# Kernel tuning notes

Hardware: AMD Instinct MI355X
Metric: run time of the kernel (lower is better)

## Reference

```python
import jax, jax.numpy as jnp
import numpy as np

N_SPK = 2048
M_UTT = 16
D_EMB = 512
EPS = 1e-8  # torch cosine_similarity eps


def setup_inputs() -> dict:
    key = jax.random.key(0)
    k1, = jax.random.split(key, 1)
    speaker_vectors = jax.random.normal(k1, (N_SPK * M_UTT, D_EMB), dtype=jnp.float32)
    return {
        "speaker_vectors": speaker_vectors,
        "w": jnp.float32(10.0),
        "b": jnp.float32(-5.0),
        "speakers": N_SPK,
    }


def _normalize(x):
    # torch.cosine_similarity clamps each norm at eps
    n = jnp.maximum(jnp.linalg.norm(x, axis=-1, keepdims=True), EPS)
    return x / n


def reference(speaker_vectors, w, b, speakers):
    N = speakers
    NM, D = speaker_vectors.shape
    M = NM // N
    v3 = speaker_vectors.reshape(N, M, D)
    ssum = v3.sum(axis=1)                         # [N, D] per-speaker sums
    C = ssum / M                                  # full centroids [N, D]
    C_min = (ssum[:, None, :] - v3) / (M - 1)     # leave-one-out centroids [N, M, D]

    vn = _normalize(speaker_vectors)              # [NM, D]
    # diagonal similarities: cos(C_min[j], v[j]) per utterance j
    S_diag = jnp.sum(_normalize(C_min.reshape(NM, D)) * vn, axis=-1)  # [NM]
    # full similarity matrix via one normalized matmul: [N, NM]
    S_full = _normalize(C) @ vn.T
    # replace each speaker's own block row entries with leave-one-out sims
    col_spk = jnp.arange(NM) // M                 # speaker id of each column
    same = col_spk[None, :] == jnp.arange(N)[:, None]  # [N, NM]
    S = jnp.where(same, S_diag[None, :], S_full)

    # L_j = -(w*S_diag_j + b) + log sum_n exp(w*S[n,j] + b)
    L = -(w * S_diag + b) + jax.nn.logsumexp(w * S + b, axis=0)
    return L.sum()
```

## Files before the change

### kernel.cpp

```cpp
#include <hip/hip_runtime.h>
#include <stdint.h>

#define N_SPK 2048
#define M_UTT 16
#define D_EMB 512
#define NM (N_SPK * M_UTT)
#define FP8_SCALE 16.0f

typedef __attribute__((ext_vector_type(4))) float f32x4;
typedef __attribute__((ext_vector_type(4))) int   i32x4;
typedef __attribute__((ext_vector_type(8))) int   i32x8;

__device__ __forceinline__ void async_copy16(const void* g, void* l) {
    __builtin_amdgcn_global_load_lds(
        (const __attribute__((address_space(1))) unsigned int*)g,
        (__attribute__((address_space(3))) unsigned int*)l,
        16, 0, 0);
}

__device__ __forceinline__ i32x8 ld_frag(const unsigned char* base, int s0) {
    i32x4 lo = *(const i32x4*)(base + s0 * 16);
    i32x4 hi = *(const i32x4*)(base + (s0 ^ 1) * 16);
    return __builtin_shufflevector(lo, hi, 0, 1, 2, 3, 4, 5, 6, 7);
}

__global__ __launch_bounds__(256) void prep_kernel(
    const float* __restrict__ V, const float* __restrict__ wp,
    const float* __restrict__ bp, unsigned char* __restrict__ Cn8,
    unsigned char* __restrict__ vn8, float* __restrict__ dterm,
    float* __restrict__ colsum, float* __restrict__ out)
{
    const int spk = blockIdx.x, t = threadIdx.x;
    const int wave = t >> 6, lane = t & 63;
    const float2* vb = (const float2*)(V + (size_t)spk * (M_UTT * D_EMB));

    __shared__ __align__(16) float red[32][264];
    __shared__ float red2[32];
    __shared__ float invs[M_UTT];
    __shared__ float wred[4];

    if (spk < 128) colsum[spk * 256 + t] = 0.f;
    if (spk == 0 && t == 0) out[0] = 0.f;

    float2 p[M_UTT];
#pragma unroll
    for (int m = 0; m < M_UTT; ++m) p[m] = vb[m * 256 + t];

    float2 ss = make_float2(0.f, 0.f);
#pragma unroll
    for (int m = 0; m < M_UTT; ++m) { ss.x += p[m].x; ss.y += p[m].y; }

    float cnp = ss.x * ss.x + ss.y * ss.y;
#pragma unroll
    for (int off = 32; off > 0; off >>= 1) cnp += __shfl_xor(cnp, off);
    if (lane == 0) wred[wave] = cnp;

#pragma unroll
    for (int m = 0; m < M_UTT; ++m) {
        red[m][t]         = ss.x * p[m].x + ss.y * p[m].y;
        red[m + M_UTT][t] = p[m].x * p[m].x + p[m].y * p[m].y;
    }
    __syncthreads();
    const float cn2 = wred[0] + wred[1] + wred[2] + wred[3];

    {
        const int r = t >> 3, s = t & 7;
        const float4* rp = (const float4*)red;
        float4 a = make_float4(0.f, 0.f, 0.f, 0.f);
#pragma unroll
        for (int k = 0; k < 8; ++k) {
            float4 q = rp[r * 66 + s + 8 * k];
            a.x += q.x; a.y += q.y; a.z += q.z; a.w += q.w;
        }
        float v1 = (a.x + a.y) + (a.z + a.w);
        v1 += __shfl_xor(v1, 1);
        v1 += __shfl_xor(v1, 2);
        v1 += __shfl_xor(v1, 4);
        if (s == 0) red2[r] = v1;
    }
    __syncthreads();

    if (t < M_UTT) {
        const float sv = red2[t], vv = red2[t + M_UTT];
        const float cc = cn2 - 2.f * sv + vv;
        const float cv = sv - vv;
        const float dc = fmaxf(sqrtf(fmaxf(cc, 0.f)) * (1.f / (M_UTT - 1)), 1e-8f) * (M_UTT - 1);
        const float dv = fmaxf(sqrtf(vv), 1e-8f);
        dterm[spk * M_UTT + t] = (*wp) * (cv / (dc * dv)) + (*bp);
        invs[t] = FP8_SCALE / dv;
    }
    __syncthreads();

    const float cs = FP8_SCALE / (M_UTT * fmaxf(sqrtf(cn2) * (1.f / M_UTT), 1e-8f));
    {
        int pk = __builtin_amdgcn_cvt_pk_fp8_f32(ss.x * cs, ss.y * cs, 0, false);
        ((unsigned short*)(Cn8 + (size_t)spk * D_EMB))[t] = (unsigned short)pk;
    }
#pragma unroll
    for (int m = 0; m < M_UTT; ++m) {
        const float iv = invs[m];
        int pk = __builtin_amdgcn_cvt_pk_fp8_f32(p[m].x * iv, p[m].y * iv, 0, false);
        ((unsigned short*)(vn8 + ((size_t)(spk * M_UTT + m)) * D_EMB))[t] = (unsigned short)pk;
    }
}

__global__ __launch_bounds__(256) void gemm_kernel(
    const unsigned char* __restrict__ Cn8, const unsigned char* __restrict__ vn8,
    const float* __restrict__ wp, const float* __restrict__ bp,
    float* __restrict__ colsum)
{
    __shared__ __align__(16) unsigned char As[128 * 256];
    __shared__ __align__(16) unsigned char Bs[128 * 256];
    __shared__ float csum[128];

    const int tid = threadIdx.x;
    const int w = tid >> 6, l = tid & 63;
    const int by = blockIdx.x;
    const int bx = blockIdx.y;
    const float wgt = (*wp) * (1.f / (FP8_SCALE * FP8_SCALE));
    const float bsc = *bp;

    if (tid < 128) csum[tid] = 0.f;

    const int r_l = l >> 4, hh = (l >> 3) & 1, sl8 = l & 7;
    const int g_even = sl8 ^ r_l;
    const size_t rowoff = (size_t)(w * 32 + r_l) * D_EMB + hh * 128;
    const unsigned char* Ab0 = Cn8 + (size_t)(by * 128) * D_EMB + rowoff + g_even * 16;
    const unsigned char* Ab1 = Cn8 + (size_t)(by * 128) * D_EMB + rowoff + (g_even ^ 4) * 16;
    const unsigned char* Bb0 = vn8 + (size_t)(bx * 128) * D_EMB + rowoff + g_even * 16;
    const unsigned char* Bb1 = vn8 + (size_t)(bx * 128) * D_EMB + rowoff + (g_even ^ 4) * 16;
    unsigned char* AsW = As + (w * 32) * 256;
    unsigned char* BsW = Bs + (w * 32) * 256;

    const int wm = w & 1, wn = w >> 1;
    const int l16 = l & 15, q = l >> 4;
    const int s0 = (2 * q) ^ (l & 7);
    const unsigned char* Ard = As + (wm * 64 + l16) * 256;
    const unsigned char* Brd = Bs + (wn * 64 + l16) * 256;

    f32x4 acc[4][4];
    const f32x4 z = {0.f, 0.f, 0.f, 0.f};
#pragma unroll
    for (int i = 0; i < 4; ++i)
#pragma unroll
        for (int j = 0; j < 4; ++j) acc[i][j] = z;

#pragma unroll
    for (int kk = 0; kk < D_EMB; kk += 256) {
        __syncthreads();
#pragma unroll
        for (int i = 0; i < 8; ++i) {
            const unsigned char* pa = ((i & 1) ? Ab1 : Ab0) + i * 2048 + kk;
            const unsigned char* pb = ((i & 1) ? Bb1 : Bb0) + i * 2048 + kk;
            async_copy16(pa, AsW + i * 1024);
            async_copy16(pb, BsW + i * 1024);
        }
        __syncthreads();
#pragma unroll
        for (int h2 = 0; h2 < 2; ++h2) {
            const int ho = h2 * 128;
            i32x8 bfr[4];
#pragma unroll
            for (int j = 0; j < 4; ++j) bfr[j] = ld_frag(Brd + j * 4096 + ho, s0);
#pragma unroll
            for (int i = 0; i < 4; ++i) {
                i32x8 af = ld_frag(Ard + i * 4096 + ho, s0);
#pragma unroll
                for (int j = 0; j < 4; ++j)
                    acc[i][j] = __builtin_amdgcn_mfma_scale_f32_16x16x128_f8f6f4(
                        af, bfr[j], acc[i][j], 0, 0, 0, 0x7F7F7F7F, 0, 0x7F7F7F7F);
            }
        }
    }

    const int rowg0 = by * 128 + wm * 64 + q * 4;
    const int colg0 = bx * 128 + wn * 64 + l16;
#pragma unroll
    for (int j = 0; j < 4; ++j) {
        const int colg = colg0 + j * 16;
        const int cspk = colg >> 4;
        float p = 0.f;
#pragma unroll
        for (int i = 0; i < 4; ++i) {
            const int rowg = rowg0 + i * 16;
#pragma unroll
            for (int r = 0; r < 4; ++r) {
                float e = __expf(wgt * acc[i][j][r] + bsc);
                p += (rowg + r == cspk) ? 0.f : e;
            }
        }
        p += __shfl_xor(p, 16);
        p += __shfl_xor(p, 32);
        if (q == 0) atomicAdd(&csum[wn * 64 + j * 16 + l16], p);
    }
    __syncthreads();
    if (tid < 128) atomicAdd(&colsum[bx * 128 + tid], csum[tid]);
}

__global__ __launch_bounds__(256) void finish_kernel(
    const float* __restrict__ dterm, const float* __restrict__ colsum,
    float* __restrict__ out)
{
    const int idx = blockIdx.x * 256 + threadIdx.x;
    const int stride = gridDim.x * 256;
    float local = 0.f;
    for (int j = idx; j < NM; j += stride) {
        float t = dterm[j];
        local += logf(colsum[j] + __expf(t)) - t;
    }
#pragma unroll
    for (int off = 32; off > 0; off >>= 1) local += __shfl_xor(local, off);
    __shared__ float wr[4];
    const int wave = threadIdx.x >> 6, lane = threadIdx.x & 63;
    if (lane == 0) wr[wave] = local;
    __syncthreads();
    if (threadIdx.x == 0) atomicAdd(out, wr[0] + wr[1] + wr[2] + wr[3]);
}

extern "C" void kernel_launch(void* const* d_in, const int* in_sizes, int n_in,
                              void* d_out, int out_size, void* d_ws, size_t ws_size,
                              hipStream_t stream) {
    const float* V  = (const float*)d_in[0];
    const float* wp = (const float*)d_in[1];
    const float* bp = (const float*)d_in[2];

    char* ws = (char*)d_ws;
    unsigned char* Cn8 = (unsigned char*)ws;
    unsigned char* vn8 = (unsigned char*)(ws + ((size_t)1 << 20));
    float* dterm  = (float*)(ws + ((size_t)17 << 20));
    float* colsum = dterm + NM;
    float* out    = (float*)d_out;

    prep_kernel<<<N_SPK, 256, 0, stream>>>(V, wp, bp, Cn8, vn8, dterm, colsum, out);
    gemm_kernel<<<dim3(N_SPK / 128, NM / 128), 256, 0, stream>>>(Cn8, vn8, wp, bp, colsum);
    finish_kernel<<<64, 256, 0, stream>>>(dterm, colsum, out);
}
```

Baseline: 149.2 us.

## Double-buffer LDS tiles along K in the FP8 GEMM kernel

The GEMM kernel now splits the 512-wide K dimension into four 128-byte stages held in two LDS buffers, instead of two 256-byte stages in a single buffer. The async global-to-LDS copy for the next stage is issued before the MFMA work on the current stage, so loads overlap with compute. The XOR swizzle is rewritten for the 128-byte row stride. In exchange there are more barrier rounds per tile, and correctness depends on the barrier also waiting for the outstanding async copies.

Result: slower. 154.8 us (+3.8%).

```diff
diff --git a/kernel.cpp b/kernel.cpp
--- a/kernel.cpp
+++ b/kernel.cpp
@@ -109,8 +109,8 @@
     const float* __restrict__ wp, const float* __restrict__ bp,
     float* __restrict__ colsum)
 {
-    __shared__ __align__(16) unsigned char As[128 * 256];
-    __shared__ __align__(16) unsigned char Bs[128 * 256];
+    __shared__ __align__(16) unsigned char As[2][128 * 128];
+    __shared__ __align__(16) unsigned char Bs[2][128 * 128];
     __shared__ float csum[128];
 
     const int tid = threadIdx.x;
@@ -122,21 +122,17 @@
 
     if (tid < 128) csum[tid] = 0.f;
 
-    const int r_l = l >> 4, hh = (l >> 3) & 1, sl8 = l & 7;
-    const int g_even = sl8 ^ r_l;
-    const size_t rowoff = (size_t)(w * 32 + r_l) * D_EMB + hh * 128;
-    const unsigned char* Ab0 = Cn8 + (size_t)(by * 128) * D_EMB + rowoff + g_even * 16;
-    const unsigned char* Ab1 = Cn8 + (size_t)(by * 128) * D_EMB + rowoff + (g_even ^ 4) * 16;
-    const unsigned char* Bb0 = vn8 + (size_t)(bx * 128) * D_EMB + rowoff + g_even * 16;
-    const unsigned char* Bb1 = vn8 + (size_t)(bx * 128) * D_EMB + rowoff + (g_even ^ 4) * 16;
-    unsigned char* AsW = As + (w * 32) * 256;
-    unsigned char* BsW = Bs + (w * 32) * 256;
+    const int srow = w * 32 + (l >> 3);
+    const int sg   = (l & 7) ^ ((l >> 3) & 7);
+    const unsigned char* Ab = Cn8 + (size_t)(by * 128 + srow) * D_EMB + sg * 16;
+    const unsigned char* Bb = vn8 + (size_t)(bx * 128 + srow) * D_EMB + sg * 16;
+    const int woff = (w * 32) * 128;
 
     const int wm = w & 1, wn = w >> 1;
     const int l16 = l & 15, q = l >> 4;
     const int s0 = (2 * q) ^ (l & 7);
-    const unsigned char* Ard = As + (wm * 64 + l16) * 256;
-    const unsigned char* Brd = Bs + (wn * 64 + l16) * 256;
+    const int rdoff = (wm * 64 + l16) * 128;
+    const int rdoffB = (wn * 64 + l16) * 128;
 
     f32x4 acc[4][4];
     const f32x4 z = {0.f, 0.f, 0.f, 0.f};
@@ -146,31 +142,37 @@
         for (int j = 0; j < 4; ++j) acc[i][j] = z;
 
 #pragma unroll
-    for (int kk = 0; kk < D_EMB; kk += 256) {
+    for (int i = 0; i < 4; ++i) {
+        async_copy16(Ab + (size_t)(i * 8) * D_EMB, &As[0][woff + i * 1024]);
+        async_copy16(Bb + (size_t)(i * 8) * D_EMB, &Bs[0][woff + i * 1024]);
+    }
+    __syncthreads();
+
+#pragma unroll
+    for (int it = 0; it < 4; ++it) {
+        const int cur = it & 1, nxt = cur ^ 1;
+        if (it < 3) {
+            const int kk = (it + 1) * 128;
+#pragma unroll
+            for (int i = 0; i < 4; ++i) {
+                async_copy16(Ab + kk + (size_t)(i * 8) * D_EMB, &As[nxt][woff + i * 1024]);
+                async_copy16(Bb + kk + (size_t)(i * 8) * D_EMB, &Bs[nxt][woff + i * 1024]);
+            }
+        }
+        const unsigned char* Ard = &As[cur][rdoff];
+        const unsigned char* Brd = &Bs[cur][rdoffB];
+        i32x8 bfr[4];
+#pragma unroll
+        for (int j = 0; j < 4; ++j) bfr[j] = ld_frag(Brd + j * 2048, s0);
+#pragma unroll
+        for (int i = 0; i < 4; ++i) {
+            i32x8 af = ld_frag(Ard + i * 2048, s0);
+#pragma unroll
+            for (int j = 0; j < 4; ++j)
+                acc[i][j] = __builtin_amdgcn_mfma_scale_f32_16x16x128_f8f6f4(
+                    af, bfr[j], acc[i][j], 0, 0, 0, 0x7F7F7F7F, 0, 0x7F7F7F7F);
+        }
         __syncthreads();
-#pragma unroll
-        for (int i = 0; i < 8; ++i) {
-            const unsigned char* pa = ((i & 1) ? Ab1 : Ab0) + i * 2048 + kk;
-            const unsigned char* pb = ((i & 1) ? Bb1 : Bb0) + i * 2048 + kk;
-            async_copy16(pa, AsW + i * 1024);
-            async_copy16(pb, BsW + i * 1024);
-        }
-        __syncthreads();
-#pragma unroll
-        for (int h2 = 0; h2 < 2; ++h2) {
-            const int ho = h2 * 128;
-            i32x8 bfr[4];
-#pragma unroll
-            for (int j = 0; j < 4; ++j) bfr[j] = ld_frag(Brd + j * 4096 + ho, s0);
-#pragma unroll
-            for (int i = 0; i < 4; ++i) {
-                i32x8 af = ld_frag(Ard + i * 4096 + ho, s0);
-#pragma unroll
-                for (int j = 0; j < 4; ++j)
-                    acc[i][j] = __builtin_amdgcn_mfma_scale_f32_16x16x128_f8f6f4(
-                        af, bfr[j], acc[i][j], 0, 0, 0, 0x7F7F7F7F, 0, 0x7F7F7F7F);
-            }
-        }
     }
 
     const int rowg0 = by * 128 + wm * 64 + q * 4;
```
